# Kernel tuning notes

Measured on AMD Instinct MI355X. Metric: run time of the kernel, lower is better.

## Reference

```python
import jax, jax.numpy as jnp
import numpy as np

N_NODES = 100000
N_EDGES = 1600000
N_GRAPHS = 4096
BN_EPS = 1e-5


def _gcn_conv(h, src, tgt, deg_inv_sqrt, W, b):
    # GCNConv with self-loops: out_i = sum_{j->i} (d_i d_j)^{-1/2} (XW)_j + d_i^{-1} (XW)_i + b
    h = h @ W                                   # [N, out]
    norm = (deg_inv_sqrt[src] * deg_inv_sqrt[tgt])[:, None]  # [E, 1]
    agg = jax.ops.segment_sum(h[src] * norm, tgt, num_segments=N_NODES)
    agg = agg + h * (deg_inv_sqrt ** 2)[:, None]  # self-loop term
    return agg + b


def _batch_norm(x, gamma, beta):
    # training-mode BatchNorm1d: batch statistics, biased variance
    mean = jnp.mean(x, axis=0)
    var = jnp.mean((x - mean) ** 2, axis=0)
    return (x - mean) * jax.lax.rsqrt(var + BN_EPS) * gamma + beta


def setup_inputs() -> dict:
    key = jax.random.key(0)
    ks = jax.random.split(key, 12)
    x = jax.random.normal(ks[0], (N_NODES, 128), dtype=jnp.float32)
    edge_index = jax.random.randint(ks[1], (2, N_EDGES), 0, N_NODES, dtype=jnp.int32)
    batch = jnp.sort(jax.random.randint(ks[2], (N_NODES,), 0, N_GRAPHS, dtype=jnp.int32))
    def lin(k, fi, fo):
        return jax.random.normal(k, (fi, fo), dtype=jnp.float32) / np.sqrt(fi)
    return {
        "x": x, "edge_index": edge_index, "batch": batch,
        "W1": lin(ks[3], 128, 128), "b1": jnp.zeros((128,), jnp.float32),
        "W2": lin(ks[4], 128, 128), "b2": jnp.zeros((128,), jnp.float32),
        "W3": lin(ks[5], 128, 256), "b3": jnp.zeros((256,), jnp.float32),
        "g1": jnp.ones((128,), jnp.float32), "be1": jnp.zeros((128,), jnp.float32),
        "g2": jnp.ones((128,), jnp.float32), "be2": jnp.zeros((128,), jnp.float32),
    }


def reference(x, edge_index, batch, W1, b1, W2, b2, W3, b3, g1, be1, g2, be2):
    src, tgt = edge_index[0], edge_index[1]
    # degrees including self-loop
    deg = jax.ops.segment_sum(jnp.ones((N_EDGES,), x.dtype), tgt, num_segments=N_NODES) + 1.0
    deg_inv_sqrt = jax.lax.rsqrt(deg)

    h = _gcn_conv(x, src, tgt, deg_inv_sqrt, W1, b1)
    h = jax.nn.relu(_batch_norm(h, g1, be1))          # dropout(p=0.1) as identity (eval)
    h = _gcn_conv(h, src, tgt, deg_inv_sqrt, W2, b2)
    h = jax.nn.relu(_batch_norm(h, g2, be2))
    h = _gcn_conv(h, src, tgt, deg_inv_sqrt, W3, b3)  # [N, 256]

    # global mean pool over batch ids
    sums = jax.ops.segment_sum(h, batch, num_segments=N_GRAPHS)
    counts = jax.ops.segment_sum(jnp.ones((N_NODES,), h.dtype), batch, num_segments=N_GRAPHS)
    return sums / jnp.maximum(counts, 1.0)[:, None]
```

## Files before the change

kernel.cpp:

```cpp
#include <hip/hip_runtime.h>
#include <hip/hip_bf16.h>

#define BN_EPS 1e-5f
#define AGG_BLOCKS 2048
#define BSHIFT 9
#define BUCKN 512
#define NBP 256
#define CB 256

static inline int cdiv(long long a, long long b) { return (int)((a + b - 1) / b); }

typedef __attribute__((ext_vector_type(8))) short short8v;
typedef __attribute__((ext_vector_type(4))) float f32x4;

__device__ __forceinline__ float lo16(int u) {
    return __uint_as_float(((unsigned int)u) << 16);
}
__device__ __forceinline__ float hi16(int u) {
    return __uint_as_float(((unsigned int)u) & 0xffff0000u);
}
__device__ __forceinline__ unsigned short f2bf(float f) {
    unsigned int b = __float_as_uint(f);
    b += 0x7FFFu + ((b >> 16) & 1u);
    return (unsigned short)(b >> 16);
}

__global__ __launch_bounds__(256) void k_bhist(const int* __restrict__ tgt,
                                               int* __restrict__ hcnt, int E, int tile,
                                               int nbuck) {
    __shared__ int lh[NBP];
    const int t = threadIdx.x;
    lh[t] = 0;
    __syncthreads();
    const int base = blockIdx.x * tile;
    const int end = min(base + tile, E);
    for (int i = base + t; i < end; i += 256)
        atomicAdd(&lh[tgt[i] >> BSHIFT], 1);
    __syncthreads();
    if (t < nbuck) hcnt[blockIdx.x * NBP + t] = lh[t];
}

__global__ __launch_bounds__(256) void k_bscan(int* __restrict__ hcnt,
                                               int* __restrict__ btot) {
    const int bucket = blockIdx.x;
    const int t = threadIdx.x;
    __shared__ int sh[256];
    int v = hcnt[t * NBP + bucket];
    sh[t] = v;
    __syncthreads();
    for (int d = 1; d < 256; d <<= 1) {
        int u = (t >= d) ? sh[t - d] : 0;
        __syncthreads();
        sh[t] += u;
        __syncthreads();
    }
    hcnt[t * NBP + bucket] = sh[t] - v;
    if (t == 255) btot[bucket] = sh[255];
}

__global__ __launch_bounds__(256) void k_scan_small(const int* __restrict__ btot,
                                                    int* __restrict__ bbase, int nb) {
    const int t = threadIdx.x;
    __shared__ int sh[256];
    int v = (t < nb) ? btot[t] : 0;
    sh[t] = v;
    __syncthreads();
    for (int d = 1; d < 256; d <<= 1) {
        int u = (t >= d) ? sh[t - d] : 0;
        __syncthreads();
        sh[t] += u;
        __syncthreads();
    }
    if (t < nb) bbase[t] = sh[t] - v;
    if (t == nb) bbase[nb] = sh[255];
    if (t == 255 && nb <= 255) bbase[nb] = sh[255];
}

__global__ __launch_bounds__(256) void k_bscatter2(const int* __restrict__ src,
                                                   const int* __restrict__ tgt,
                                                   const int* __restrict__ hcnt,
                                                   const int* __restrict__ bbase,
                                                   int2* __restrict__ pairs, int E,
                                                   int tile, int nbuck) {
    __shared__ int cur[NBP];
    const int t = threadIdx.x;
    if (t < nbuck) cur[t] = bbase[t] + hcnt[blockIdx.x * NBP + t];
    __syncthreads();
    const int base = blockIdx.x * tile;
    const int end = min(base + tile, E);
    for (int i = base + t; i < end; i += 256) {
        int s = src[i];
        int tg = tgt[i];
        int p = atomicAdd(&cur[tg >> BSHIFT], 1);
        pairs[p] = make_int2(s, tg);
    }
}

__global__ __launch_bounds__(256) void k_bucket_csr(const int2* __restrict__ pairs,
                                                    const int* __restrict__ bbase,
                                                    int* __restrict__ roff,
                                                    float* __restrict__ dis,
                                                    int* __restrict__ esrc,
                                                    int N, int nbuck,
                                                    const int* __restrict__ batch,
                                                    int* __restrict__ goff, int G) {
    const int t = threadIdx.x;
    if ((int)blockIdx.x >= nbuck) {
        int i = (blockIdx.x - nbuck) * 256 + t;
        if (i >= N) return;
        int cur = batch[i];
        int prev = (i == 0) ? -1 : batch[i - 1];
        for (int g = prev + 1; g <= cur; g++) goff[g] = i;
        if (i == N - 1) {
            for (int g = cur + 1; g <= G; g++) goff[g] = N;
        }
        return;
    }
    __shared__ int cnt[BUCKN];
    __shared__ int cur[BUCKN];
    __shared__ int sh[256];
    const int b = blockIdx.x;
    const int nb0 = b * BUCKN;
    cnt[t] = 0;
    cnt[t + 256] = 0;
    __syncthreads();
    const int lo = bbase[b], hi = bbase[b + 1];
    for (int p = lo + t; p < hi; p += 256)
        atomicAdd(&cnt[pairs[p].y - nb0], 1);
    __syncthreads();
    const int c0 = cnt[2 * t], c1 = cnt[2 * t + 1];
    int s = c0 + c1;
    sh[t] = s;
    __syncthreads();
    for (int d = 1; d < 256; d <<= 1) {
        int u = (t >= d) ? sh[t - d] : 0;
        __syncthreads();
        sh[t] += u;
        __syncthreads();
    }
    const int excl = sh[t] - s + lo;
    cur[2 * t] = excl;
    cur[2 * t + 1] = excl + c0;
    const int n0 = nb0 + 2 * t, n1 = n0 + 1;
    if (n0 < N) { roff[n0] = excl; dis[n0] = rsqrtf((float)c0 + 1.0f); }
    if (n1 < N) { roff[n1] = excl + c0; dis[n1] = rsqrtf((float)c1 + 1.0f); }
    if (b == nbuck - 1 && t == 0) roff[N] = hi;
    __syncthreads();
    for (int p = lo + t; p < hi; p += 256) {
        int2 e = pairs[p];
        int q = atomicAdd(&cur[e.y - nb0], 1);
        esrc[q] = e.x;
    }
}

template <bool BN>
__global__ __launch_bounds__(256) void k_gemm_mfma(const float* __restrict__ X,
                                                   const float* __restrict__ W,
                                                   unsigned short* __restrict__ Y, int N,
                                                   const float* __restrict__ dis,
                                                   const float* __restrict__ sums,
                                                   const float* __restrict__ sumsq,
                                                   const float* __restrict__ g,
                                                   const float* __restrict__ be,
                                                   float inv_n) {
    __shared__ unsigned short As[64][136];
    __shared__ unsigned short Bs[64][136];
    const int t = threadIdx.x;
    const int rbase = blockIdx.x * 64;
    const int cbase = blockIdx.y * 64;

    for (int it = 0; it < 8; it++) {
        int idx = t + it * 256;
        int r = idx >> 5;
        int k4 = (idx & 31) * 4;
        int row = rbase + r;
        float4 v = make_float4(0.f, 0.f, 0.f, 0.f);
        if (row < N) v = *(const float4*)(X + (size_t)row * 128 + k4);
        float o[4] = {v.x, v.y, v.z, v.w};
        if (BN) {
#pragma unroll
            for (int j = 0; j < 4; j++) {
                int c = k4 + j;
                float mean = sums[c] * inv_n;
                float var = sumsq[c] * inv_n - mean * mean;
                float sc = rsqrtf(var + BN_EPS) * g[c];
                o[j] = fmaxf((o[j] - mean) * sc + be[c], 0.0f);
            }
        }
        ushort4 u;
        u.x = f2bf(o[0]); u.y = f2bf(o[1]); u.z = f2bf(o[2]); u.w = f2bf(o[3]);
        *(ushort4*)&As[r][k4] = u;
    }
    for (int it = 0; it < 8; it++) {
        int idx = t + it * 256;
        int k = idx >> 4;
        int c4 = (idx & 15) * 4;
        float4 v = *(const float4*)(W + (size_t)k * 128 + cbase + c4);
        Bs[c4 + 0][k] = f2bf(v.x);
        Bs[c4 + 1][k] = f2bf(v.y);
        Bs[c4 + 2][k] = f2bf(v.z);
        Bs[c4 + 3][k] = f2bf(v.w);
    }
    __syncthreads();

    const int wid = t >> 6;
    const int lane = t & 63;
    const int wr = (wid >> 1) * 32;
    const int wc = (wid & 1) * 32;
    const int lrow = lane & 15;
    const int lkg = lane >> 4;

    f32x4 acc00 = 0, acc01 = 0, acc10 = 0, acc11 = 0;
#pragma unroll
    for (int kk = 0; kk < 4; kk++) {
        const int k0 = kk * 32 + lkg * 8;
        short8v a0 = *(const short8v*)&As[wr + lrow][k0];
        short8v a1 = *(const short8v*)&As[wr + 16 + lrow][k0];
        short8v b0 = *(const short8v*)&Bs[wc + lrow][k0];
        short8v b1 = *(const short8v*)&Bs[wc + 16 + lrow][k0];
        acc00 = __builtin_amdgcn_mfma_f32_16x16x32_bf16(a0, b0, acc00, 0, 0, 0);
        acc01 = __builtin_amdgcn_mfma_f32_16x16x32_bf16(a0, b1, acc01, 0, 0, 0);
        acc10 = __builtin_amdgcn_mfma_f32_16x16x32_bf16(a1, b0, acc10, 0, 0, 0);
        acc11 = __builtin_amdgcn_mfma_f32_16x16x32_bf16(a1, b1, acc11, 0, 0, 0);
    }

#pragma unroll
    for (int rt = 0; rt < 2; rt++) {
        const f32x4 va = rt ? acc10 : acc00;
        const f32x4 vb = rt ? acc11 : acc01;
#pragma unroll
        for (int reg = 0; reg < 4; reg++) {
            int row = rbase + wr + rt * 16 + lkg * 4 + reg;
            if (row < N) {
                float dv = dis[row];
                Y[(size_t)row * 128 + cbase + wc + lrow] = f2bf(va[reg] * dv);
                Y[(size_t)row * 128 + cbase + wc + 16 + lrow] = f2bf(vb[reg] * dv);
            }
        }
    }
}

__global__ __launch_bounds__(256) void k_gemm_final(const float* __restrict__ X,
                                                    const float* __restrict__ W,
                                                    const float* __restrict__ bias,
                                                    const int* __restrict__ goff,
                                                    float* __restrict__ out, int G) {
    __shared__ float xt[128][64];
    __shared__ float wt[128][64];
    const int t = threadIdx.x;
    const int rbase = blockIdx.x * 64;
    const int cbase = blockIdx.y * 64;

    for (int it = 0; it < 8; it++) {
        int idx = t + it * 256;
        int k4 = idx >> 6;
        int r = idx & 63;
        int row = rbase + r;
        float4 v = make_float4(0.f, 0.f, 0.f, 0.f);
        if (row < G) v = *(const float4*)(X + (size_t)row * 128 + k4 * 4);
        xt[k4 * 4 + 0][r] = v.x;
        xt[k4 * 4 + 1][r] = v.y;
        xt[k4 * 4 + 2][r] = v.z;
        xt[k4 * 4 + 3][r] = v.w;
    }
    for (int it = 0; it < 8; it++) {
        int idx = t + it * 256;
        int k = idx >> 4;
        int c4 = (idx & 15) * 4;
        *(float4*)&wt[k][c4] = *(const float4*)(W + (size_t)k * 256 + cbase + c4);
    }
    __syncthreads();

    const int r0 = (t >> 4) * 4;
    const int c0 = (t & 15) * 4;
    float acc[4][4];
#pragma unroll
    for (int i = 0; i < 4; i++)
#pragma unroll
        for (int j = 0; j < 4; j++) acc[i][j] = 0.0f;

#pragma unroll 4
    for (int k = 0; k < 128; k++) {
        float4 a = *(const float4*)&xt[k][r0];
        float4 b = *(const float4*)&wt[k][c0];
        const float av[4] = {a.x, a.y, a.z, a.w};
        const float bv[4] = {b.x, b.y, b.z, b.w};
#pragma unroll
        for (int i = 0; i < 4; i++)
#pragma unroll
            for (int j = 0; j < 4; j++) acc[i][j] += av[i] * bv[j];
    }

#pragma unroll
    for (int i = 0; i < 4; i++) {
        int row = rbase + r0 + i;
        if (row < G) {
            bool empty = (goff[row + 1] == goff[row]);
            float4 o;
            o.x = empty ? 0.f : acc[i][0] + bias[cbase + c0 + 0];
            o.y = empty ? 0.f : acc[i][1] + bias[cbase + c0 + 1];
            o.z = empty ? 0.f : acc[i][2] + bias[cbase + c0 + 2];
            o.w = empty ? 0.f : acc[i][3] + bias[cbase + c0 + 3];
            *(float4*)(out + (size_t)row * 256 + cbase + c0) = o;
        }
    }
}

template <bool STATS>
__global__ __launch_bounds__(256) void k_aggr2(const unsigned short* __restrict__ H,
                                               const int* __restrict__ esrc,
                                               const int* __restrict__ roff,
                                               const float* __restrict__ dis,
                                               const float* __restrict__ bias,
                                               float* __restrict__ out, int N,
                                               float* __restrict__ partial) {
    constexpr int M = 128;
    constexpr int GSZ = 16;
    constexpr int GPB = 16;
    const int nGroups = gridDim.x * GPB;
    const int gid = blockIdx.x * GPB + threadIdx.x / GSZ;
    const int lane = threadIdx.x % GSZ;
    const int c8 = lane * 8;
    float4 bva = make_float4(0.f, 0.f, 0.f, 0.f);
    float4 bvb = make_float4(0.f, 0.f, 0.f, 0.f);
    if (bias) {
        bva = *(const float4*)(bias + c8);
        bvb = *(const float4*)(bias + c8 + 4);
    }

    float ss[8], sq[8];
    if (STATS) {
#pragma unroll
        for (int k = 0; k < 8; k++) { ss[k] = 0.f; sq[k] = 0.f; }
    }

    for (int n = gid; n < N; n += nGroups) {
        const int rs = roff[n], re = roff[n + 1];
        float acc[8];
#pragma unroll
        for (int j = 0; j < 8; j++) acc[j] = 0.0f;

        int e = rs;
        for (; e + 8 <= re; e += 8) {
            int sid[8];
#pragma unroll
            for (int q = 0; q < 8; q++) sid[q] = esrc[e + q];
            int4 hv[8];
#pragma unroll
            for (int q = 0; q < 8; q++)
                hv[q] = *(const int4*)(H + (size_t)sid[q] * M + c8);
#pragma unroll
            for (int q = 0; q < 8; q++) {
                const int w[4] = {hv[q].x, hv[q].y, hv[q].z, hv[q].w};
#pragma unroll
                for (int k = 0; k < 4; k++) {
                    acc[2 * k + 0] += lo16(w[k]);
                    acc[2 * k + 1] += hi16(w[k]);
                }
            }
        }
        if (e + 4 <= re) {
            int sid[4];
#pragma unroll
            for (int q = 0; q < 4; q++) sid[q] = esrc[e + q];
            int4 hv[4];
#pragma unroll
            for (int q = 0; q < 4; q++)
                hv[q] = *(const int4*)(H + (size_t)sid[q] * M + c8);
#pragma unroll
            for (int q = 0; q < 4; q++) {
                const int w[4] = {hv[q].x, hv[q].y, hv[q].z, hv[q].w};
#pragma unroll
                for (int k = 0; k < 4; k++) {
                    acc[2 * k + 0] += lo16(w[k]);
                    acc[2 * k + 1] += hi16(w[k]);
                }
            }
            e += 4;
        }
        for (; e < re; e++) {
            const int s = esrc[e];
            const int4 h = *(const int4*)(H + (size_t)s * M + c8);
            const int w[4] = {h.x, h.y, h.z, h.w};
#pragma unroll
            for (int k = 0; k < 4; k++) {
                acc[2 * k + 0] += lo16(w[k]);
                acc[2 * k + 1] += hi16(w[k]);
            }
        }
        {
            const int4 h = *(const int4*)(H + (size_t)n * M + c8);
            const int w[4] = {h.x, h.y, h.z, h.w};
#pragma unroll
            for (int k = 0; k < 4; k++) {
                acc[2 * k + 0] += lo16(w[k]);
                acc[2 * k + 1] += hi16(w[k]);
            }
        }
        const float dn = dis[n];
        float ov[8];
#pragma unroll
        for (int k = 0; k < 8; k++) {
            float b = (k < 4) ? (&bva.x)[k] : (&bvb.x)[k - 4];
            ov[k] = acc[k] * dn + b;
            if (STATS) { ss[k] += ov[k]; sq[k] += ov[k] * ov[k]; }
        }
        float4 oa = make_float4(ov[0], ov[1], ov[2], ov[3]);
        float4 ob = make_float4(ov[4], ov[5], ov[6], ov[7]);
        *(float4*)(out + (size_t)n * M + c8) = oa;
        *(float4*)(out + (size_t)n * M + c8 + 4) = ob;
    }

    if (STATS) {
        __shared__ float ls[GPB][256];
        const int g = threadIdx.x / GSZ;
#pragma unroll
        for (int k = 0; k < 8; k++) {
            ls[g][c8 + k] = ss[k];
            ls[g][128 + c8 + k] = sq[k];
        }
        __syncthreads();
        const int f = threadIdx.x;
        float v = 0.f;
#pragma unroll
        for (int gg = 0; gg < GPB; gg++) v += ls[gg][f];
        partial[(size_t)blockIdx.x * 256 + f] = v;
    }
}

__global__ __launch_bounds__(256) void k_redstats(const float* __restrict__ partial,
                                                  float* __restrict__ sums,
                                                  float* __restrict__ sumsq, int nblk) {
    const int f = blockIdx.x;
    const int t = threadIdx.x;
    float v = 0.f;
    for (int b = t; b < nblk; b += 256) v += partial[(size_t)b * 256 + f];
    __shared__ float sh[256];
    sh[t] = v;
    __syncthreads();
    for (int d = 128; d > 0; d >>= 1) {
        if (t < d) sh[t] += sh[t + d];
        __syncthreads();
    }
    if (t == 0) {
        if (f < 128) sums[f] = sh[0];
        else sumsq[f - 128] = sh[0];
    }
}

__global__ void k_bncast(const float* __restrict__ X, const float* __restrict__ sums,
                         const float* __restrict__ sumsq, const float* __restrict__ g,
                         const float* __restrict__ be, const float* __restrict__ dis,
                         unsigned short* __restrict__ Y, long long total4, float inv_n) {
    long long idx = (long long)blockIdx.x * blockDim.x + threadIdx.x;
    if (idx >= total4) return;
    int c4 = ((int)idx & 31) << 2;
    const float dn = dis[(int)(idx >> 5)];
    float4 v = *(const float4*)(X + idx * 4);
    float o[4] = {v.x, v.y, v.z, v.w};
    ushort4 r;
    unsigned short* rp = &r.x;
#pragma unroll
    for (int j = 0; j < 4; j++) {
        int c = c4 + j;
        float mean = sums[c] * inv_n;
        float var = sumsq[c] * inv_n - mean * mean;
        float sc = rsqrtf(var + BN_EPS) * g[c];
        rp[j] = f2bf(fmaxf((o[j] - mean) * sc + be[c], 0.0f) * dn);
    }
    *(ushort4*)(Y + idx * 4) = r;
}

__global__ void k_pool_seg(const float* __restrict__ H, const int* __restrict__ goff,
                           float* __restrict__ out) {
    const int gr = blockIdx.x;
    const int c = threadIdx.x;
    const int s = goff[gr], e = goff[gr + 1];
    float acc = 0.0f;
    for (int i = s; i < e; i++) acc += H[(size_t)i * 128 + c];
    out[(size_t)gr * 128 + c] = acc / fmaxf((float)(e - s), 1.0f);
}

extern "C" void kernel_launch(void* const* d_in, const int* in_sizes, int n_in,
                              void* d_out, int out_size, void* d_ws, size_t ws_size,
                              hipStream_t stream) {
    const float* x     = (const float*)d_in[0];
    const int*   ei    = (const int*)d_in[1];
    const int*   batch = (const int*)d_in[2];
    const float* W1 = (const float*)d_in[3];
    const float* b1 = (const float*)d_in[4];
    const float* W2 = (const float*)d_in[5];
    const float* b2 = (const float*)d_in[6];
    const float* W3 = (const float*)d_in[7];
    const float* b3 = (const float*)d_in[8];
    const float* g1 = (const float*)d_in[9];
    const float* be1 = (const float*)d_in[10];
    const float* g2 = (const float*)d_in[11];
    const float* be2 = (const float*)d_in[12];
    float* out = (float*)d_out;

    const int N = in_sizes[2];
    const int E = in_sizes[1] / 2;
    const int G = out_size / 256;
    const int* src = ei;
    const int* tgt = ei + E;

    char* ws = (char*)d_ws;
    auto take = [&](size_t bytes) {
        char* p = ws;
        ws += (bytes + 255) & ~(size_t)255;
        return p;
    };
    float*          bufB   = (float*)take((size_t)N * 128 * 4);
    unsigned short* bufH   = (unsigned short*)take((size_t)N * 128 * 2);
    float*          P      = (float*)take((size_t)G * 128 * 4);
    float*          dis    = (float*)take((size_t)N * 4);
    float*          sums   = (float*)take(512 * 4);
    float*          sumsq  = sums + 128;
    float*          partial= (float*)take((size_t)AGG_BLOCKS * 256 * 4);
    int*            roff   = (int*)take((size_t)(N + 1) * 4);
    int*            esrc   = (int*)take((size_t)E * 4);
    int*            goff   = (int*)take((size_t)(G + 1) * 4);
    int*            hcnt   = (int*)take((size_t)CB * NBP * 4);
    int*            btot   = (int*)take(NBP * 4);
    int*            bbase  = (int*)take((NBP + 1) * 4);
    int2*           pairs  = (int2*)bufB;

    const int B = 256;
    const int nbuck = cdiv(N, BUCKN);
    const int tile = cdiv(E, CB);

    k_bhist<<<CB, B, 0, stream>>>(tgt, hcnt, E, tile, nbuck);
    k_bscan<<<nbuck, B, 0, stream>>>(hcnt, btot);
    k_scan_small<<<1, B, 0, stream>>>(btot, bbase, nbuck);
    k_bscatter2<<<CB, B, 0, stream>>>(src, tgt, hcnt, bbase, pairs, E, tile, nbuck);
    k_bucket_csr<<<nbuck + cdiv(N, B), B, 0, stream>>>(pairs, bbase, roff, dis, esrc,
                                                       N, nbuck, batch, goff, G);

    long long t4_128 = (long long)N * 32;
    const int nbx = cdiv(N, 64);

    k_gemm_mfma<false><<<dim3(nbx, 2), B, 0, stream>>>(x, W1, bufH, N, dis,
                                                       nullptr, nullptr, nullptr, nullptr, 0.f);
    k_aggr2<true><<<AGG_BLOCKS, B, 0, stream>>>(bufH, esrc, roff, dis, b1, bufB, N, partial);
    k_redstats<<<256, B, 0, stream>>>(partial, sums, sumsq, AGG_BLOCKS);

    k_gemm_mfma<true><<<dim3(nbx, 2), B, 0, stream>>>(bufB, W2, bufH, N, dis,
                                                      sums, sumsq, g1, be1, 1.0f / N);
    k_aggr2<true><<<AGG_BLOCKS, B, 0, stream>>>(bufH, esrc, roff, dis, b2, bufB, N, partial);
    k_redstats<<<256, B, 0, stream>>>(partial, sums, sumsq, AGG_BLOCKS);

    k_bncast<<<cdiv(t4_128, B), B, 0, stream>>>(bufB, sums, sumsq, g2, be2, dis, bufH,
                                                t4_128, 1.0f / N);
    k_aggr2<false><<<AGG_BLOCKS, B, 0, stream>>>(bufH, esrc, roff, dis, nullptr, bufB, N, nullptr);
    k_pool_seg<<<G, 128, 0, stream>>>(bufB, goff, P);
    k_gemm_final<<<dim3(cdiv(G, 64), 4), B, 0, stream>>>(P, W3, b3, goff, out, G);
}
```

Before: 361.5 us.

## Store aggregation outputs in bf16 and fuse final aggregation with mean pooling

New measurement: 340.6 us. 1.06x faster.

```diff
diff --git a/kernel.cpp b/kernel.cpp
--- a/kernel.cpp
+++ b/kernel.cpp
@@ -13,6 +13,9 @@
 typedef __attribute__((ext_vector_type(8))) short short8v;
 typedef __attribute__((ext_vector_type(4))) float f32x4;
 
+__device__ __forceinline__ float bf2f(unsigned short u) {
+    return __uint_as_float(((unsigned int)u) << 16);
+}
 __device__ __forceinline__ float lo16(int u) {
     return __uint_as_float(((unsigned int)u) << 16);
 }
@@ -23,6 +26,9 @@
     unsigned int b = __float_as_uint(f);
     b += 0x7FFFu + ((b >> 16) & 1u);
     return (unsigned short)(b >> 16);
+}
+__device__ __forceinline__ int pack2bf(float a, float b) {
+    return (int)f2bf(a) | ((int)f2bf(b) << 16);
 }
 
 __global__ __launch_bounds__(256) void k_bhist(const int* __restrict__ tgt,
@@ -154,7 +160,7 @@
 }
 
 template <bool BN>
-__global__ __launch_bounds__(256) void k_gemm_mfma(const float* __restrict__ X,
+__global__ __launch_bounds__(256) void k_gemm_mfma(const void* __restrict__ Xv,
                                                    const float* __restrict__ W,
                                                    unsigned short* __restrict__ Y, int N,
                                                    const float* __restrict__ dis,
@@ -174,9 +180,18 @@
         int r = idx >> 5;
         int k4 = (idx & 31) * 4;
         int row = rbase + r;
-        float4 v = make_float4(0.f, 0.f, 0.f, 0.f);
-        if (row < N) v = *(const float4*)(X + (size_t)row * 128 + k4);
-        float o[4] = {v.x, v.y, v.z, v.w};
+        float o[4] = {0.f, 0.f, 0.f, 0.f};
+        if (row < N) {
+            if constexpr (BN) {
+                const unsigned short* Xb = (const unsigned short*)Xv;
+                ushort4 uv = *(const ushort4*)(Xb + (size_t)row * 128 + k4);
+                o[0] = bf2f(uv.x); o[1] = bf2f(uv.y); o[2] = bf2f(uv.z); o[3] = bf2f(uv.w);
+            } else {
+                const float* Xf = (const float*)Xv;
+                float4 v = *(const float4*)(Xf + (size_t)row * 128 + k4);
+                o[0] = v.x; o[1] = v.y; o[2] = v.z; o[3] = v.w;
+            }
+        }
         if (BN) {
 #pragma unroll
             for (int j = 0; j < 4; j++) {
@@ -306,13 +321,78 @@
     }
 }
 
-template <bool STATS>
+__device__ __forceinline__ void gather_row(const unsigned short* __restrict__ H,
+                                           const int* __restrict__ esrc,
+                                           int rs, int re, int n, int c8,
+                                           float (&acc)[8]) {
+    constexpr int M = 128;
+#pragma unroll
+    for (int j = 0; j < 8; j++) acc[j] = 0.0f;
+    int e = rs;
+    for (; e + 8 <= re; e += 8) {
+        int sid[8];
+#pragma unroll
+        for (int q = 0; q < 8; q++) sid[q] = esrc[e + q];
+        int4 hv[8];
+#pragma unroll
+        for (int q = 0; q < 8; q++)
+            hv[q] = *(const int4*)(H + (size_t)sid[q] * M + c8);
+#pragma unroll
+        for (int q = 0; q < 8; q++) {
+            const int w[4] = {hv[q].x, hv[q].y, hv[q].z, hv[q].w};
+#pragma unroll
+            for (int k = 0; k < 4; k++) {
+                acc[2 * k + 0] += lo16(w[k]);
+                acc[2 * k + 1] += hi16(w[k]);
+            }
+        }
+    }
+    if (e + 4 <= re) {
+        int sid[4];
+#pragma unroll
+        for (int q = 0; q < 4; q++) sid[q] = esrc[e + q];
+        int4 hv[4];
+#pragma unroll
+        for (int q = 0; q < 4; q++)
+            hv[q] = *(const int4*)(H + (size_t)sid[q] * M + c8);
+#pragma unroll
+        for (int q = 0; q < 4; q++) {
+            const int w[4] = {hv[q].x, hv[q].y, hv[q].z, hv[q].w};
+#pragma unroll
+            for (int k = 0; k < 4; k++) {
+                acc[2 * k + 0] += lo16(w[k]);
+                acc[2 * k + 1] += hi16(w[k]);
+            }
+        }
+        e += 4;
+    }
+    for (; e < re; e++) {
+        const int s = esrc[e];
+        const int4 h = *(const int4*)(H + (size_t)s * M + c8);
+        const int w[4] = {h.x, h.y, h.z, h.w};
+#pragma unroll
+        for (int k = 0; k < 4; k++) {
+            acc[2 * k + 0] += lo16(w[k]);
+            acc[2 * k + 1] += hi16(w[k]);
+        }
+    }
+    {
+        const int4 h = *(const int4*)(H + (size_t)n * M + c8);
+        const int w[4] = {h.x, h.y, h.z, h.w};
+#pragma unroll
+        for (int k = 0; k < 4; k++) {
+            acc[2 * k + 0] += lo16(w[k]);
+            acc[2 * k + 1] += hi16(w[k]);
+        }
+    }
+}
+
 __global__ __launch_bounds__(256) void k_aggr2(const unsigned short* __restrict__ H,
                                                const int* __restrict__ esrc,
                                                const int* __restrict__ roff,
                                                const float* __restrict__ dis,
                                                const float* __restrict__ bias,
-                                               float* __restrict__ out, int N,
+                                               unsigned short* __restrict__ out, int N,
                                                float* __restrict__ partial) {
     constexpr int M = 128;
     constexpr int GSZ = 16;
@@ -321,110 +401,82 @@
     const int gid = blockIdx.x * GPB + threadIdx.x / GSZ;
     const int lane = threadIdx.x % GSZ;
     const int c8 = lane * 8;
-    float4 bva = make_float4(0.f, 0.f, 0.f, 0.f);
-    float4 bvb = make_float4(0.f, 0.f, 0.f, 0.f);
-    if (bias) {
-        bva = *(const float4*)(bias + c8);
-        bvb = *(const float4*)(bias + c8 + 4);
-    }
+    const float4 bva = *(const float4*)(bias + c8);
+    const float4 bvb = *(const float4*)(bias + c8 + 4);
 
     float ss[8], sq[8];
-    if (STATS) {
-#pragma unroll
-        for (int k = 0; k < 8; k++) { ss[k] = 0.f; sq[k] = 0.f; }
-    }
+#pragma unroll
+    for (int k = 0; k < 8; k++) { ss[k] = 0.f; sq[k] = 0.f; }
 
     for (int n = gid; n < N; n += nGroups) {
-        const int rs = roff[n], re = roff[n + 1];
         float acc[8];
-#pragma unroll
-        for (int j = 0; j < 8; j++) acc[j] = 0.0f;
-
-        int e = rs;
-        for (; e + 8 <= re; e += 8) {
-            int sid[8];
-#pragma unroll
-            for (int q = 0; q < 8; q++) sid[q] = esrc[e + q];
-            int4 hv[8];
-#pragma unroll
-            for (int q = 0; q < 8; q++)
-                hv[q] = *(const int4*)(H + (size_t)sid[q] * M + c8);
-#pragma unroll
-            for (int q = 0; q < 8; q++) {
-                const int w[4] = {hv[q].x, hv[q].y, hv[q].z, hv[q].w};
-#pragma unroll
-                for (int k = 0; k < 4; k++) {
-                    acc[2 * k + 0] += lo16(w[k]);
-                    acc[2 * k + 1] += hi16(w[k]);
-                }
-            }
-        }
-        if (e + 4 <= re) {
-            int sid[4];
-#pragma unroll
-            for (int q = 0; q < 4; q++) sid[q] = esrc[e + q];
-            int4 hv[4];
-#pragma unroll
-            for (int q = 0; q < 4; q++)
-                hv[q] = *(const int4*)(H + (size_t)sid[q] * M + c8);
-#pragma unroll
-            for (int q = 0; q < 4; q++) {
-                const int w[4] = {hv[q].x, hv[q].y, hv[q].z, hv[q].w};
-#pragma unroll
-                for (int k = 0; k < 4; k++) {
-                    acc[2 * k + 0] += lo16(w[k]);
-                    acc[2 * k + 1] += hi16(w[k]);
-                }
-            }
-            e += 4;
-        }
-        for (; e < re; e++) {
-            const int s = esrc[e];
-            const int4 h = *(const int4*)(H + (size_t)s * M + c8);
-            const int w[4] = {h.x, h.y, h.z, h.w};
-#pragma unroll
-            for (int k = 0; k < 4; k++) {
-                acc[2 * k + 0] += lo16(w[k]);
-                acc[2 * k + 1] += hi16(w[k]);
-            }
-        }
-        {
-            const int4 h = *(const int4*)(H + (size_t)n * M + c8);
-            const int w[4] = {h.x, h.y, h.z, h.w};
-#pragma unroll
-            for (int k = 0; k < 4; k++) {
-                acc[2 * k + 0] += lo16(w[k]);
-                acc[2 * k + 1] += hi16(w[k]);
-            }
-        }
+        gather_row(H, esrc, roff[n], roff[n + 1], n, c8, acc);
         const float dn = dis[n];
         float ov[8];
 #pragma unroll
         for (int k = 0; k < 8; k++) {
             float b = (k < 4) ? (&bva.x)[k] : (&bvb.x)[k - 4];
             ov[k] = acc[k] * dn + b;
-            if (STATS) { ss[k] += ov[k]; sq[k] += ov[k] * ov[k]; }
-        }
-        float4 oa = make_float4(ov[0], ov[1], ov[2], ov[3]);
-        float4 ob = make_float4(ov[4], ov[5], ov[6], ov[7]);
-        *(float4*)(out + (size_t)n * M + c8) = oa;
-        *(float4*)(out + (size_t)n * M + c8 + 4) = ob;
-    }
-
-    if (STATS) {
-        __shared__ float ls[GPB][256];
-        const int g = threadIdx.x / GSZ;
-#pragma unroll
-        for (int k = 0; k < 8; k++) {
-            ls[g][c8 + k] = ss[k];
-            ls[g][128 + c8 + k] = sq[k];
-        }
-        __syncthreads();
-        const int f = threadIdx.x;
+            ss[k] += ov[k];
+            sq[k] += ov[k] * ov[k];
+        }
+        int4 o;
+        o.x = pack2bf(ov[0], ov[1]);
+        o.y = pack2bf(ov[2], ov[3]);
+        o.z = pack2bf(ov[4], ov[5]);
+        o.w = pack2bf(ov[6], ov[7]);
+        *(int4*)(out + (size_t)n * M + c8) = o;
+    }
+
+    __shared__ float ls[GPB][256];
+    const int g = threadIdx.x / GSZ;
+#pragma unroll
+    for (int k = 0; k < 8; k++) {
+        ls[g][c8 + k] = ss[k];
+        ls[g][128 + c8 + k] = sq[k];
+    }
+    __syncthreads();
+    const int f = threadIdx.x;
+    float v = 0.f;
+#pragma unroll
+    for (int gg = 0; gg < GPB; gg++) v += ls[gg][f];
+    partial[(size_t)blockIdx.x * 256 + f] = v;
+}
+
+__global__ __launch_bounds__(256) void k_aggr_pool(const unsigned short* __restrict__ H,
+                                                   const int* __restrict__ esrc,
+                                                   const int* __restrict__ roff,
+                                                   const float* __restrict__ dis,
+                                                   const int* __restrict__ goff,
+                                                   float* __restrict__ P) {
+    const int gr = blockIdx.x;
+    const int t = threadIdx.x;
+    const int grp = t >> 4;
+    const int lane = t & 15;
+    const int c8 = lane * 8;
+    const int s = goff[gr], e = goff[gr + 1];
+
+    float pool[8];
+#pragma unroll
+    for (int k = 0; k < 8; k++) pool[k] = 0.f;
+
+    for (int n = s + grp; n < e; n += 16) {
+        float acc[8];
+        gather_row(H, esrc, roff[n], roff[n + 1], n, c8, acc);
+        const float dn = dis[n];
+#pragma unroll
+        for (int k = 0; k < 8; k++) pool[k] += acc[k] * dn;
+    }
+
+    __shared__ float ls[16][128];
+#pragma unroll
+    for (int k = 0; k < 8; k++) ls[grp][c8 + k] = pool[k];
+    __syncthreads();
+    if (t < 128) {
         float v = 0.f;
 #pragma unroll
-        for (int gg = 0; gg < GPB; gg++) v += ls[gg][f];
-        partial[(size_t)blockIdx.x * 256 + f] = v;
+        for (int gg = 0; gg < 16; gg++) v += ls[gg][t];
+        P[(size_t)gr * 128 + t] = v / fmaxf((float)(e - s), 1.0f);
     }
 }
 
@@ -448,37 +500,37 @@
     }
 }
 
-__global__ void k_bncast(const float* __restrict__ X, const float* __restrict__ sums,
+__global__ void k_bncast(const unsigned short* __restrict__ X,
+                         const float* __restrict__ sums,
                          const float* __restrict__ sumsq, const float* __restrict__ g,
                          const float* __restrict__ be, const float* __restrict__ dis,
-                         unsigned short* __restrict__ Y, long long total4, float inv_n) {
+                         unsigned short* __restrict__ Y, long long total8, float inv_n) {
     long long idx = (long long)blockIdx.x * blockDim.x + threadIdx.x;
-    if (idx >= total4) return;
-    int c4 = ((int)idx & 31) << 2;
-    const float dn = dis[(int)(idx >> 5)];
-    float4 v = *(const float4*)(X + idx * 4);
-    float o[4] = {v.x, v.y, v.z, v.w};
-    ushort4 r;
-    unsigned short* rp = &r.x;
-#pragma unroll
-    for (int j = 0; j < 4; j++) {
-        int c = c4 + j;
+    if (idx >= total8) return;
+    int c8 = ((int)idx & 15) << 3;
+    const float dn = dis[(int)(idx >> 4)];
+    int4 v = *(const int4*)(X + idx * 8);
+    const int w[4] = {v.x, v.y, v.z, v.w};
+    float o[8];
+#pragma unroll
+    for (int k = 0; k < 4; k++) {
+        o[2 * k + 0] = lo16(w[k]);
+        o[2 * k + 1] = hi16(w[k]);
+    }
+#pragma unroll
+    for (int j = 0; j < 8; j++) {
+        int c = c8 + j;
         float mean = sums[c] * inv_n;
         float var = sumsq[c] * inv_n - mean * mean;
         float sc = rsqrtf(var + BN_EPS) * g[c];
-        rp[j] = f2bf(fmaxf((o[j] - mean) * sc + be[c], 0.0f) * dn);
-    }
-    *(ushort4*)(Y + idx * 4) = r;
-}
-
-__global__ void k_pool_seg(const float* __restrict__ H, const int* __restrict__ goff,
-                           float* __restrict__ out) {
-    const int gr = blockIdx.x;
-    const int c = threadIdx.x;
-    const int s = goff[gr], e = goff[gr + 1];
-    float acc = 0.0f;
-    for (int i = s; i < e; i++) acc += H[(size_t)i * 128 + c];
-    out[(size_t)gr * 128 + c] = acc / fmaxf((float)(e - s), 1.0f);
+        o[j] = fmaxf((o[j] - mean) * sc + be[c], 0.0f) * dn;
+    }
+    int4 r;
+    r.x = pack2bf(o[0], o[1]);
+    r.y = pack2bf(o[2], o[3]);
+    r.z = pack2bf(o[4], o[5]);
+    r.w = pack2bf(o[6], o[7]);
+    *(int4*)(Y + idx * 8) = r;
 }
 
 extern "C" void kernel_launch(void* const* d_in, const int* in_sizes, int n_in,
@@ -511,7 +563,7 @@
         ws += (bytes + 255) & ~(size_t)255;
         return p;
     };
-    float*          bufB   = (float*)take((size_t)N * 128 * 4);
+    unsigned short* bufB   = (unsigned short*)take((size_t)N * 128 * 2);
     unsigned short* bufH   = (unsigned short*)take((size_t)N * 128 * 2);
     float*          P      = (float*)take((size_t)G * 128 * 4);
     float*          dis    = (float*)take((size_t)N * 4);
@@ -524,7 +576,7 @@
     int*            hcnt   = (int*)take((size_t)CB * NBP * 4);
     int*            btot   = (int*)take(NBP * 4);
     int*            bbase  = (int*)take((NBP + 1) * 4);
-    int2*           pairs  = (int2*)bufB;
+    int2*           pairs  = (int2*)take((size_t)E * 8);
 
     const int B = 256;
     const int nbuck = cdiv(N, BUCKN);
@@ -537,22 +589,21 @@
     k_bucket_csr<<<nbuck + cdiv(N, B), B, 0, stream>>>(pairs, bbase, roff, dis, esrc,
                                                        N, nbuck, batch, goff, G);
 
-    long long t4_128 = (long long)N * 32;
+    long long t8_128 = (long long)N * 16;
     const int nbx = cdiv(N, 64);
 
     k_gemm_mfma<false><<<dim3(nbx, 2), B, 0, stream>>>(x, W1, bufH, N, dis,
                                                        nullptr, nullptr, nullptr, nullptr, 0.f);
-    k_aggr2<true><<<AGG_BLOCKS, B, 0, stream>>>(bufH, esrc, roff, dis, b1, bufB, N, partial);
+    k_aggr2<<<AGG_BLOCKS, B, 0, stream>>>(bufH, esrc, roff, dis, b1, bufB, N, partial);
     k_redstats<<<256, B, 0, stream>>>(partial, sums, sumsq, AGG_BLOCKS);
 
     k_gemm_mfma<true><<<dim3(nbx, 2), B, 0, stream>>>(bufB, W2, bufH, N, dis,
                                                       sums, sumsq, g1, be1, 1.0f / N);
-    k_aggr2<true><<<AGG_BLOCKS, B, 0, stream>>>(bufH, esrc, roff, dis, b2, bufB, N, partial);
+    k_aggr2<<<AGG_BLOCKS, B, 0, stream>>>(bufH, esrc, roff, dis, b2, bufB, N, partial);
     k_redstats<<<256, B, 0, stream>>>(partial, sums, sumsq, AGG_BLOCKS);
 
-    k_bncast<<<cdiv(t4_128, B), B, 0, stream>>>(bufB, sums, sumsq, g2, be2, dis, bufH,
-                                                t4_128, 1.0f / N);
-    k_aggr2<false><<<AGG_BLOCKS, B, 0, stream>>>(bufH, esrc, roff, dis, nullptr, bufB, N, nullptr);
-    k_pool_seg<<<G, 128, 0, stream>>>(bufB, goff, P);
+    k_bncast<<<cdiv(t8_128, B), B, 0, stream>>>(bufB, sums, sumsq, g2, be2, dis, bufH,
+                                                t8_128, 1.0f / N);
+    k_aggr_pool<<<G, B, 0, stream>>>(bufH, esrc, roff, dis, goff, P);
     k_gemm_final<<<dim3(cdiv(G, 64), 4), B, 0, stream>>>(P, W3, b3, goff, out, G);
 }
```
